# Optimization experiments

Hardware: AMD Instinct MI355X
Metric: run time of the kernel (lower is better)

## Reference

```python
import jax, jax.numpy as jnp
import numpy as np

B, N, D, H, K, L, BLOCKS = 8, 256, 768, 12, 128, 4, 2
HD = D // H
SCALING = HD ** -0.5
NEG = -1e9  # stand-in for -inf; exp underflows to exactly 0 in softmax


def layernorm(x, s, b):
    m = x.mean(-1, keepdims=True)
    v = ((x - m) ** 2).mean(-1, keepdims=True)
    return (x - m) * jax.lax.rsqrt(v + 1e-5) * s + b


def _gauss(x, mean, std):
    a = (2.0 * 3.14159) ** 0.5
    return jnp.exp(-0.5 * ((x - mean) / std) ** 2) / (a * std)


def setup_inputs() -> dict:
    key = jax.random.key(0)
    ks = jax.random.split(key, 16)
    nrm = lambda k, shape: jax.random.normal(k, shape, jnp.float32) * 0.02
    atoms = jax.random.randint(ks[0], (B, N), 0, 10, dtype=jnp.int32)
    pos = jax.random.normal(ks[1], (B, N, 3), jnp.float32)
    atom_emb = nrm(ks[2], (10, D)).at[0].set(0.0)  # padding_idx=0
    gbf_means = jax.random.uniform(ks[3], (K,), jnp.float32, 0.0, 3.0)
    gbf_stds = jax.random.uniform(ks[4], (K,), jnp.float32, 0.0, 3.0)
    gbf_mul = jnp.ones((100, 1), jnp.float32)
    gbf_bias = jnp.zeros((100, 1), jnp.float32)
    bp_w1 = nrm(ks[5], (K, K)); bp_b1 = jnp.zeros((K,), jnp.float32)
    bp_w2 = nrm(ks[6], (K, H)); bp_b2 = jnp.zeros((H,), jnp.float32)
    edge_w = nrm(ks[7], (K, D)); edge_b = jnp.zeros((D,), jnp.float32)
    ap_w = nrm(ks[8], (D, D)); ap_b = jnp.zeros((D,), jnp.float32)
    ln1_s = jnp.ones((L, D), jnp.float32); ln1_b = jnp.zeros((L, D), jnp.float32)
    wi = nrm(ks[9], (L, D, 3 * D)); bi = jnp.zeros((L, 3 * D), jnp.float32)
    wo = nrm(ks[10], (L, D, D)); bo = jnp.zeros((L, D), jnp.float32)
    ln2_s = jnp.ones((L, D), jnp.float32); ln2_b = jnp.zeros((L, D), jnp.float32)
    w1 = nrm(ks[11], (L, D, D)); b1 = jnp.zeros((L, D), jnp.float32)
    w2 = nrm(ks[12], (L, D, D)); b2 = jnp.zeros((L, D), jnp.float32)
    fln_s = jnp.ones((D,), jnp.float32); fln_b = jnp.zeros((D,), jnp.float32)
    return dict(atoms=atoms, pos=pos, atom_emb=atom_emb, gbf_means=gbf_means,
                gbf_stds=gbf_stds, gbf_mul=gbf_mul, gbf_bias=gbf_bias,
                bp_w1=bp_w1, bp_b1=bp_b1, bp_w2=bp_w2, bp_b2=bp_b2,
                edge_w=edge_w, edge_b=edge_b, ap_w=ap_w, ap_b=ap_b,
                ln1_s=ln1_s, ln1_b=ln1_b, wi=wi, bi=bi, wo=wo, bo=bo,
                ln2_s=ln2_s, ln2_b=ln2_b, w1=w1, b1=b1, w2=w2, b2=b2,
                fln_s=fln_s, fln_b=fln_b)


def reference(atoms, pos, atom_emb, gbf_means, gbf_stds, gbf_mul, gbf_bias,
              bp_w1, bp_b1, bp_w2, bp_b2, edge_w, edge_b, ap_w, ap_b,
              ln1_s, ln1_b, wi, bi, wo, bo, ln2_s, ln2_b, w1, b1, w2, b2,
              fln_s, fln_b):
    pad = atoms == 0  # [B,N]
    delta = pos[:, None, :, :] - pos[:, :, None, :]  # [B,N,N,3]
    sq = (delta * delta).sum(-1)
    dist = jnp.where(sq > 0, jnp.sqrt(jnp.where(sq > 0, sq, 1.0)), 0.0)  # safe sqrt
    et = atoms[:, :, None] * 10 + atoms[:, None, :]  # [B,N,N] in [0,100)
    e = gbf_mul[et] * dist[..., None] + gbf_bias[et]  # [B,N,N,1]
    gbf = _gauss(e, gbf_means, jnp.abs(gbf_stds) + 1e-5)  # [B,N,N,K]
    # zero out padded j-columns, sum over j -> per-node edge feature
    ef = jnp.where(pad[:, None, :, None], 0.0, gbf).sum(axis=2)  # [B,N,K]
    node = atom_emb[atoms] + ef @ edge_w + edge_b  # [B,N,D]
    x = jnp.swapaxes(node, 0, 1) @ ap_w + ap_b  # [N,B,D]
    # attention bias: K-dim Gaussian features -> per-head bias
    bias = jax.nn.gelu(gbf @ bp_w1 + bp_b1, approximate=False) @ bp_w2 + bp_b2  # [B,N,N,H]
    bias = jnp.transpose(bias, (0, 3, 1, 2))  # [B,H,N,N]
    bias = jnp.where(pad[:, None, None, :], NEG, bias)

    def body(x, p):
        s1, c1, Wi, Bi, Wo, Bo, s2, c2, W1, B1, W2, B2 = p
        h = layernorm(x, s1, c1)
        q, k, v = jnp.split(h @ Wi + Bi, 3, axis=-1)
        q = q.reshape(N, B, H, HD) * SCALING
        k = k.reshape(N, B, H, HD)
        v = v.reshape(N, B, H, HD)
        sc = jnp.einsum('ibhd,jbhd->bhij', q, k) + bias
        pA = jax.nn.softmax(sc, axis=-1)
        o = jnp.einsum('bhij,jbhd->ibhd', pA, v).reshape(N, B, D)
        x = x + o @ Wo + Bo
        h = layernorm(x, s2, c2)
        h = jax.nn.gelu(h @ W1 + B1, approximate=False) @ W2 + B2
        return x + h, None

    stacked = (ln1_s, ln1_b, wi, bi, wo, bo, ln2_s, ln2_b, w1, b1, w2, b2)
    for _ in range(BLOCKS):
        x, _ = jax.lax.scan(body, x, stacked)
    x = layernorm(x, fln_s, fln_b)
    return jnp.swapaxes(x, 0, 1)  # [B,N,D]
```

## Files before the change

### kernel.cpp

```cpp
#include <hip/hip_runtime.h>
#include <math.h>

constexpr int Bn = 8, Nn = 256, Dn = 768, Hn = 12, Kn = 128;
constexpr int Tn = Nn * Bn;
constexpr float SCALE = 0.125f;
constexpr float NEGB = -1e9f;
constexpr float INV768 = 1.0f / 768.0f;

typedef __attribute__((ext_vector_type(8))) short bf16x8;
typedef __attribute__((ext_vector_type(4))) float f32x4;

#define MFMA16(a, b, c) __builtin_amdgcn_mfma_f32_16x16x32_bf16((a), (b), (c), 0, 0, 0)

__device__ __forceinline__ void gload_lds16(const void* g, void* l) {
  __builtin_amdgcn_global_load_lds(
      (const __attribute__((address_space(1))) void*)g,
      (__attribute__((address_space(3))) void*)l, 16, 0, 0);
}

__device__ __forceinline__ ushort f2bf(float x) {
  union { float f; unsigned u; } v; v.f = x;
  unsigned r = (v.u + 0x7fff + ((v.u >> 16) & 1)) >> 16;
  return (ushort)r;
}
__device__ __forceinline__ ushort f2bf_t(float x) {
  union { float f; unsigned u; } v; v.f = x;
  return (ushort)(v.u >> 16);
}
__device__ __forceinline__ float bf2f(ushort u) {
  union { unsigned u; float f; } v; v.u = ((unsigned)u) << 16;
  return v.f;
}
__device__ __forceinline__ unsigned pk2(float a, float b) {
  return (unsigned)f2bf_t(a) | ((unsigned)f2bf_t(b) << 16);
}
__device__ __forceinline__ float gelu_fast(float x) {
  float u = x * (0.7978845608f + 0.0356774081f * x * x);
  float e = __expf(2.0f * u);
  float t = 1.0f - 2.0f / (e + 1.0f);
  return 0.5f * x * (1.0f + t);
}
__device__ __forceinline__ float wave_sum(float v) {
#pragma unroll
  for (int off = 32; off; off >>= 1) v += __shfl_xor(v, off);
  return v;
}

__global__ __launch_bounds__(256) void wtrans(const float* __restrict__ W,
                                              ushort* __restrict__ WT,
                                              int Kd, int Nd) {
  __shared__ float tile[64][65];
  const float* Wl = W + (size_t)blockIdx.z * Kd * Nd;
  ushort* WTl = WT + (size_t)blockIdx.z * Kd * Nd;
  int n0 = blockIdx.x * 64, k0 = blockIdx.y * 64;
  int tid = threadIdx.x;
  for (int e = tid; e < 64 * 64; e += 256) {
    int r = e >> 6, c = e & 63;
    tile[r][c] = Wl[(size_t)(k0 + r) * Nd + n0 + c];
  }
  __syncthreads();
  for (int e = tid; e < 64 * 64; e += 256) {
    int r = e >> 6, c = e & 63;
    WTl[(size_t)(n0 + r) * Kd + k0 + c] = f2bf(tile[c][r]);
  }
}

__global__ __launch_bounds__(256) void gbias_kernel(
    const int* __restrict__ atoms, const float* __restrict__ pos,
    const float* __restrict__ means, const float* __restrict__ stds,
    const float* __restrict__ gmul, const float* __restrict__ gbias_,
    const ushort* __restrict__ w1T, const float* __restrict__ b1,
    const float* __restrict__ w2, const float* __restrict__ b2,
    ushort* __restrict__ biasb, ushort* __restrict__ efb) {
  int i = blockIdx.x, b = blockIdx.y;
  __shared__ char W1s[32768];
  __shared__ char Ag[16384];
  __shared__ char W2s[4096];
  __shared__ float sj[256];
  __shared__ int pml[256];
  __shared__ float b1s[128], kA[128], kB[128], kC[128], kcns[128];
  const int tid = threadIdx.x, w = tid >> 6, ln = tid & 63;
  const int frow = ln & 15, fgrp = ln >> 4;
  {
    int srow = ln >> 4, sc = ln & 15;
#pragma unroll
    for (int q = 0; q < 8; ++q) {
      int inst = w * 8 + q;
      int row = inst * 4 + srow;
      const char* g = (const char*)(w1T + row * 128) + ((sc * 16) ^ ((row & 7) << 4));
      gload_lds16(g, W1s + inst * 1024);
    }
  }
  if (tid < 128) {
    float mean = means[tid];
    float sd = fabsf(stds[tid]) + 1e-5f;
    float inv = 1.0f / sd;
    float A = -0.5f * inv * inv;
    kA[tid] = A;
    kB[tid] = -2.0f * A * mean;
    kC[tid] = A * mean * mean;
    kcns[tid] = inv * 0.3989423f;
    b1s[tid] = b1[tid];
  }
  for (int e = tid; e < 2048; e += 256) {
    int h = e >> 7, k = e & 127;
    float v = (h < 12) ? w2[k * 12 + h] : 0.f;
    *(ushort*)(W2s + h * 256 + ((2 * k) ^ ((h & 7) << 4))) = f2bf(v);
  }
  {
    int ai = atoms[b * Nn + i];
    int j = tid;
    int aj = atoms[b * Nn + j];
    float dx = pos[(b * Nn + i) * 3]     - pos[(b * Nn + j) * 3];
    float dy = pos[(b * Nn + i) * 3 + 1] - pos[(b * Nn + j) * 3 + 1];
    float dz = pos[(b * Nn + i) * 3 + 2] - pos[(b * Nn + j) * 3 + 2];
    float sq = dx * dx + dy * dy + dz * dz;
    float d = sq > 0.f ? sqrtf(sq) : 0.f;
    int et = ai * 10 + aj;
    sj[j] = fmaf(gmul[et], d, gbias_[et]);
    pml[j] = (aj == 0);
  }
  __syncthreads();

  const int kp = tid & 63, rquad = tid >> 6;
  const int k0i = 2 * kp, k1i = 2 * kp + 1;
  const float A0 = kA[k0i], B0 = kB[k0i], C0 = kC[k0i], cn0 = kcns[k0i];
  const float A1 = kA[k1i], B1 = kB[k1i], C1 = kC[k1i], cn1 = kcns[k1i];
  float facc0 = 0.f, facc1 = 0.f;

  for (int jt = 0; jt < 4; ++jt) {
    int j0 = jt * 64;
#pragma unroll
    for (int rr = 0; rr < 16; ++rr) {
      int row = rquad * 16 + rr;
      int jg = j0 + row;
      float s = sj[jg];
      float e0 = __expf(fmaf(fmaf(A0, s, B0), s, C0));
      float e1 = __expf(fmaf(fmaf(A1, s, B1), s, C1));
      int padj = pml[jg];
      facc0 += padj ? 0.f : e0;
      facc1 += padj ? 0.f : e1;
      *(unsigned*)(Ag + row * 256 + ((4 * kp) ^ ((row & 7) << 4))) = pk2(e0 * cn0, e1 * cn1);
    }
    __syncthreads();
    f32x4 acc[8] = {};
    const int arow = w * 16 + frow;
#pragma unroll
    for (int ks = 0; ks < 4; ++ks) {
      bf16x8 af = *(const bf16x8*)(Ag + arow * 256 + ((ks * 64 + fgrp * 16) ^ ((arow & 7) << 4)));
#pragma unroll
      for (int nt = 0; nt < 8; ++nt) {
        int brow = nt * 16 + frow;
        bf16x8 bfv = *(const bf16x8*)(W1s + brow * 256 + ((ks * 64 + fgrp * 16) ^ ((brow & 7) << 4)));
        acc[nt] = MFMA16(af, bfv, acc[nt]);
      }
    }
    __syncthreads();
#pragma unroll
    for (int nt = 0; nt < 8; ++nt) {
      int n = nt * 16 + frow;
#pragma unroll
      for (int r = 0; r < 4; ++r) {
        int jloc = w * 16 + fgrp * 4 + r;
        float g = gelu_fast(acc[nt][r] + b1s[n]);
        *(ushort*)(Ag + jloc * 256 + ((2 * n) ^ ((jloc & 7) << 4))) = f2bf_t(g);
      }
    }
    __syncthreads();
    {
      f32x4 acc2 = {};
      int jrow = w * 16 + frow;
#pragma unroll
      for (int ks = 0; ks < 4; ++ks) {
        bf16x8 af = *(const bf16x8*)(Ag + jrow * 256 + ((ks * 64 + fgrp * 16) ^ ((jrow & 7) << 4)));
        bf16x8 bfv = *(const bf16x8*)(W2s + frow * 256 + ((ks * 64 + fgrp * 16) ^ ((frow & 7) << 4)));
        acc2 = MFMA16(af, bfv, acc2);
      }
      if (frow < 12) {
        float bv = b2[frow];
#pragma unroll
        for (int r = 0; r < 4; ++r) {
          int jl = w * 16 + fgrp * 4 + r;
          int jg = j0 + jl;
          float v = pml[jg] ? NEGB : (acc2[r] + bv);
          biasb[(((size_t)b * Hn + frow) * Nn + i) * Nn + jg] = f2bf(v);
        }
      }
    }
    __syncthreads();
  }
  {
    float* efp = (float*)Ag;
    efp[(kp * 4 + rquad) * 2 + 0] = facc0;
    efp[(kp * 4 + rquad) * 2 + 1] = facc1;
    __syncthreads();
    if (tid < 128) {
      int k = tid, kq = k >> 1, lo = k & 1;
      float s = efp[(kq * 4 + 0) * 2 + lo] + efp[(kq * 4 + 1) * 2 + lo] +
                efp[(kq * 4 + 2) * 2 + lo] + efp[(kq * 4 + 3) * 2 + lo];
      efb[(size_t)(b * Nn + i) * Kn + k] = f2bf(s * kcns[k]);
    }
  }
}

template <int MODE>
__global__ __launch_bounds__(256, 4) void mgemm(
    const ushort* __restrict__ A, const ushort* __restrict__ WT,
    const float* __restrict__ bias, const float* __restrict__ res,
    void* __restrict__ Cout, const int* __restrict__ atomsp,
    const float* __restrict__ embp, int M, int Kd, int Nd) {
  __shared__ char smem[16384];
  char* ldsA = smem;
  char* ldsB = smem + 8192;
  const int tid = threadIdx.x, w = tid >> 6, ln = tid & 63;
  const int m0 = blockIdx.y * 64, n0 = blockIdx.x * 64;
  const int wm = (w >> 1) * 32, wn = (w & 1) * 32;
  const int srow = ln >> 3, schunk = ln & 7;
  const int sswz = (schunk * 16) ^ (srow << 4);
  const int frow = ln & 15, fgrp = ln >> 4;
  f32x4 acc[2][2] = {};
  for (int kt = 0; kt < Kd; kt += 64) {
    __syncthreads();
#pragma unroll
    for (int q = 0; q < 2; ++q) {
      int r = (w * 2 + q) * 8 + srow;
      gload_lds16((const char*)(A + (size_t)(m0 + r) * Kd + kt) + sswz, ldsA + (w * 2 + q) * 1024);
    }
#pragma unroll
    for (int q = 0; q < 2; ++q) {
      int r = (w * 2 + q) * 8 + srow;
      gload_lds16((const char*)(WT + (size_t)(n0 + r) * Kd + kt) + sswz, ldsB + (w * 2 + q) * 1024);
    }
    __syncthreads();
#pragma unroll
    for (int ks = 0; ks < 2; ++ks) {
      bf16x8 af[2], bfv[2];
#pragma unroll
      for (int mt = 0; mt < 2; ++mt) {
        int row = wm + mt * 16 + frow;
        af[mt] = *(const bf16x8*)(ldsA + row * 128 + ((ks * 64 + fgrp * 16) ^ ((row & 7) << 4)));
      }
#pragma unroll
      for (int nt = 0; nt < 2; ++nt) {
        int row = wn + nt * 16 + frow;
        bfv[nt] = *(const bf16x8*)(ldsB + row * 128 + ((ks * 64 + fgrp * 16) ^ ((row & 7) << 4)));
      }
      acc[0][0] = MFMA16(af[0], bfv[0], acc[0][0]);
      acc[0][1] = MFMA16(af[0], bfv[1], acc[0][1]);
      acc[1][0] = MFMA16(af[1], bfv[0], acc[1][0]);
      acc[1][1] = MFMA16(af[1], bfv[1], acc[1][1]);
    }
  }
#pragma unroll
  for (int nt = 0; nt < 2; ++nt) {
    int n = n0 + wn + nt * 16 + frow;
    float bv = bias[n];
#pragma unroll
    for (int mt = 0; mt < 2; ++mt) {
#pragma unroll
      for (int r = 0; r < 4; ++r) {
        int m = m0 + wm + mt * 16 + fgrp * 4 + r;
        float v = acc[mt][nt][r] + bv;
        if (MODE == 1) v = gelu_fast(v);
        if (MODE == 2) v += res[(size_t)m * Nd + n];
        if (MODE == 5) v += embp[(size_t)atomsp[m] * Nd + n];
        if (MODE == 2 || MODE == 3) ((float*)Cout)[(size_t)m * Nd + n] = v;
        else                        ((ushort*)Cout)[(size_t)m * Nd + n] = f2bf(v);
      }
    }
  }
}

__global__ __launch_bounds__(256, 2) void mgemm128_qkv(
    const ushort* __restrict__ A, const ushort* __restrict__ WT,
    const float* __restrict__ bias, ushort* __restrict__ vTout,
    ushort* __restrict__ Cout, int M, int Kd, int Nd) {
  __shared__ char smem[32768];
  char* ldsA = smem;
  char* ldsB = smem + 16384;
  const int tid = threadIdx.x, w = tid >> 6, ln = tid & 63;
  const int m0 = blockIdx.y * 128, n0 = blockIdx.x * 128;
  const int wm = (w >> 1) * 64, wn = (w & 1) * 64;
  const int srow = ln >> 3, schunk = ln & 7;
  const int sswz = (schunk * 16) ^ (srow << 4);
  const int frow = ln & 15, fgrp = ln >> 4;
  f32x4 acc[4][4] = {};
  for (int kt = 0; kt < Kd; kt += 64) {
    __syncthreads();
#pragma unroll
    for (int q = 0; q < 4; ++q) {
      int r = (w * 4 + q) * 8 + srow;
      gload_lds16((const char*)(A + (size_t)(m0 + r) * Kd + kt) + sswz, ldsA + (w * 4 + q) * 1024);
    }
#pragma unroll
    for (int q = 0; q < 4; ++q) {
      int r = (w * 4 + q) * 8 + srow;
      gload_lds16((const char*)(WT + (size_t)(n0 + r) * Kd + kt) + sswz, ldsB + (w * 4 + q) * 1024);
    }
    __syncthreads();
#pragma unroll
    for (int ks = 0; ks < 2; ++ks) {
      bf16x8 af[4], bfv[4];
#pragma unroll
      for (int mt = 0; mt < 4; ++mt) {
        int row = wm + mt * 16 + frow;
        af[mt] = *(const bf16x8*)(ldsA + row * 128 + ((ks * 64 + fgrp * 16) ^ ((row & 7) << 4)));
      }
#pragma unroll
      for (int nt = 0; nt < 4; ++nt) {
        int row = wn + nt * 16 + frow;
        bfv[nt] = *(const bf16x8*)(ldsB + row * 128 + ((ks * 64 + fgrp * 16) ^ ((row & 7) << 4)));
      }
#pragma unroll
      for (int mt = 0; mt < 4; ++mt)
#pragma unroll
        for (int nt = 0; nt < 4; ++nt)
          acc[mt][nt] = MFMA16(af[mt], bfv[nt], acc[mt][nt]);
    }
  }
#pragma unroll
  for (int nt = 0; nt < 4; ++nt) {
    int n = n0 + wn + nt * 16 + frow;
    float bv = bias[n];
    if (n >= 1536) {
      int dd = n - 1536, h = dd >> 6, d = dd & 63;
#pragma unroll
      for (int mt = 0; mt < 4; ++mt) {
#pragma unroll
        for (int r = 0; r < 4; ++r) {
          int m = m0 + wm + mt * 16 + fgrp * 4 + r;
          int bb = m >> 8, j = m & 255;
          vTout[(((size_t)bb * Hn + h) * 64 + d) * 256 + j] = f2bf(acc[mt][nt][r] + bv);
        }
      }
    } else {
      float sc = (n < 768) ? SCALE : 1.0f;
#pragma unroll
      for (int mt = 0; mt < 4; ++mt) {
#pragma unroll
        for (int r = 0; r < 4; ++r) {
          int m = m0 + wm + mt * 16 + fgrp * 4 + r;
          Cout[(size_t)m * Nd + n] = f2bf((acc[mt][nt][r] + bv) * sc);
        }
      }
    }
  }
}

__global__ __launch_bounds__(256, 2) void attn_mfma(
    const ushort* __restrict__ qkv, const ushort* __restrict__ vT,
    const ushort* __restrict__ biasb, ushort* __restrict__ Oout) {
  int it = blockIdx.x, h = blockIdx.y, b = blockIdx.z;
  int i0 = it * 64;
  __shared__ char smem[65536];
  char* Ks = smem;
  char* Vs = smem + 32768;
  const int tid = threadIdx.x, w = tid >> 6, ln = tid & 63;
  const int frow = ln & 15, fgrp = ln >> 4;
  {
    const int srow = ln >> 3, schunk = ln & 7;
#pragma unroll
    for (int q = 0; q < 8; ++q) {
      int inst = w * 8 + q;
      int row = inst * 8 + srow;
      const char* g = (const char*)(qkv + (size_t)(b * Nn + row) * 2304 + 768 + h * 64) +
                      ((schunk * 16) ^ ((row & 7) << 4));
      gload_lds16(g, Ks + inst * 1024);
    }
#pragma unroll
    for (int q = 0; q < 8; ++q) {
      int inst = w * 8 + q;
      int row = inst * 2 + (ln >> 5);
      int cb = (ln & 31) * 16;
      const char* g = (const char*)(vT + (size_t)((b * Hn + h) * 64 + row) * 256) +
                      (cb ^ ((row & 7) << 4));
      gload_lds16(g, Vs + inst * 1024);
    }
  }
  bf16x8 qf[2];
  {
    int qrow = i0 + w * 16 + frow;
    const ushort* qg = qkv + (size_t)(b * Nn + qrow) * 2304 + h * 64 + fgrp * 8;
    qf[0] = *(const bf16x8*)qg;
    qf[1] = *(const bf16x8*)(qg + 32);
  }
  __syncthreads();
  f32x4 s[16];
#pragma unroll
  for (int jtl = 0; jtl < 16; ++jtl) {
    int row = jtl * 16 + frow;
    const char* kb = Ks + row * 128;
    bf16x8 k0 = *(const bf16x8*)(kb + ((fgrp * 16) ^ ((row & 7) << 4)));
    bf16x8 k1 = *(const bf16x8*)(kb + ((64 + fgrp * 16) ^ ((row & 7) << 4)));
    f32x4 t = {};
    t = MFMA16(qf[0], k0, t);
    t = MFMA16(qf[1], k1, t);
    s[jtl] = t;
  }
  float inv[4];
#pragma unroll
  for (int r = 0; r < 4; ++r) {
    int i = i0 + w * 16 + fgrp * 4 + r;
    const ushort* brow = biasb + (((size_t)b * Hn + h) * Nn + i) * Nn;
    float su = 0.f;
#pragma unroll
    for (int jtl = 0; jtl < 16; ++jtl) {
      float p = __expf(s[jtl][r] + bf2f(brow[jtl * 16 + frow]));
      s[jtl][r] = p;
      su += p;
    }
    su += __shfl_xor(su, 1); su += __shfl_xor(su, 2);
    su += __shfl_xor(su, 4); su += __shfl_xor(su, 8);
    inv[r] = 1.0f / su;
  }
  __syncthreads();
  char* Ps = Ks + w * 8192;
#pragma unroll
  for (int r = 0; r < 4; ++r) {
    int prow = fgrp * 4 + r;
#pragma unroll
    for (int jtl = 0; jtl < 16; ++jtl) {
      int cb = jtl * 32 + frow * 2;
      *(ushort*)(Ps + prow * 512 + (cb ^ ((prow & 7) << 4))) = f2bf_t(s[jtl][r]);
    }
  }
  __syncthreads();
  bf16x8 pf[8];
#pragma unroll
  for (int ks = 0; ks < 8; ++ks)
    pf[ks] = *(const bf16x8*)(Ps + frow * 512 + ((ks * 64 + fgrp * 16) ^ ((frow & 7) << 4)));
  f32x4 o[4] = {};
#pragma unroll
  for (int dt = 0; dt < 4; ++dt) {
#pragma unroll
    for (int ks = 0; ks < 8; ++ks) {
      int row = dt * 16 + frow;
      bf16x8 vf = *(const bf16x8*)(Vs + row * 512 + ((ks * 64 + fgrp * 16) ^ ((row & 7) << 4)));
      o[dt] = MFMA16(pf[ks], vf, o[dt]);
    }
  }
#pragma unroll
  for (int dt = 0; dt < 4; ++dt)
#pragma unroll
    for (int r = 0; r < 4; ++r) {
      int i = i0 + w * 16 + fgrp * 4 + r;
      Oout[(size_t)(b * Nn + i) * Dn + h * 64 + dt * 16 + frow] = f2bf(o[dt][r] * inv[r]);
    }
}

template <int MODE>
__global__ __launch_bounds__(256) void ln_kernel(
    const float* __restrict__ x, const float* __restrict__ sc,
    const float* __restrict__ bi, void* __restrict__ out) {
  int t = blockIdx.x;
  int tid = threadIdx.x;
  const float* xr = x + (size_t)t * Dn;
  float v0 = xr[tid], v1 = xr[tid + 256], v2 = xr[tid + 512];
  __shared__ float red[4], red2[4];
  float s = wave_sum(v0 + v1 + v2);
  if ((tid & 63) == 0) red[tid >> 6] = s;
  __syncthreads();
  float mean = (red[0] + red[1] + red[2] + red[3]) * INV768;
  float d0 = v0 - mean, d1 = v1 - mean, d2 = v2 - mean;
  float vs = wave_sum(d0 * d0 + d1 * d1 + d2 * d2);
  if ((tid & 63) == 0) red2[tid >> 6] = vs;
  __syncthreads();
  float var = (red2[0] + red2[1] + red2[2] + red2[3]) * INV768;
  float r = rsqrtf(var + 1e-5f);
  if (MODE == 0) {
    ushort* o = (ushort*)out + (size_t)t * Dn;
    o[tid]       = f2bf(d0 * r * sc[tid]       + bi[tid]);
    o[tid + 256] = f2bf(d1 * r * sc[tid + 256] + bi[tid + 256]);
    o[tid + 512] = f2bf(d2 * r * sc[tid + 512] + bi[tid + 512]);
  } else {
    float* o = (float*)out + (size_t)t * Dn;
    o[tid]       = d0 * r * sc[tid]       + bi[tid];
    o[tid + 256] = d1 * r * sc[tid + 256] + bi[tid + 256];
    o[tid + 512] = d2 * r * sc[tid + 512] + bi[tid + 512];
  }
}

extern "C" void kernel_launch(void* const* d_in, const int* in_sizes, int n_in,
                              void* d_out, int out_size, void* d_ws, size_t ws_size,
                              hipStream_t stream) {
  (void)in_sizes; (void)n_in; (void)out_size; (void)ws_size;
  const int*   atoms    = (const int*)  d_in[0];
  const float* pos      = (const float*)d_in[1];
  const float* atom_emb = (const float*)d_in[2];
  const float* gbf_means= (const float*)d_in[3];
  const float* gbf_stds = (const float*)d_in[4];
  const float* gbf_mul  = (const float*)d_in[5];
  const float* gbf_bias = (const float*)d_in[6];
  const float* bp_w1    = (const float*)d_in[7];
  const float* bp_b1    = (const float*)d_in[8];
  const float* bp_w2    = (const float*)d_in[9];
  const float* bp_b2    = (const float*)d_in[10];
  const float* edge_w   = (const float*)d_in[11];
  const float* edge_b   = (const float*)d_in[12];
  const float* ap_w     = (const float*)d_in[13];
  const float* ap_b     = (const float*)d_in[14];
  const float* ln1_s    = (const float*)d_in[15];
  const float* ln1_b    = (const float*)d_in[16];
  const float* wi       = (const float*)d_in[17];
  const float* bi       = (const float*)d_in[18];
  const float* wo       = (const float*)d_in[19];
  const float* bo       = (const float*)d_in[20];
  const float* ln2_s    = (const float*)d_in[21];
  const float* ln2_b    = (const float*)d_in[22];
  const float* w1       = (const float*)d_in[23];
  const float* b1       = (const float*)d_in[24];
  const float* w2       = (const float*)d_in[25];
  const float* b2       = (const float*)d_in[26];
  const float* fln_s    = (const float*)d_in[27];
  const float* fln_b    = (const float*)d_in[28];
  float* out = (float*)d_out;

  ushort* wsb   = (ushort*)d_ws;
  ushort* biasb = wsb;
  ushort* qkvb  = biasb + (size_t)Bn * Hn * Nn * Nn;
  ushort* hb    = qkvb + (size_t)Tn * 2304;
  ushort* vT    = hb + (size_t)Tn * Dn;
  ushort* wiT   = vT + (size_t)Bn * Hn * 64 * 256;
  ushort* woT   = wiT + (size_t)4 * 2304 * Dn;
  ushort* w1T   = woT + (size_t)4 * Dn * Dn;
  ushort* w2T   = w1T + (size_t)4 * Dn * Dn;
  ushort* w1bT  = w2T + (size_t)4 * Dn * Dn;
  float*  xbuf  = (float*)(w1bT + 16384);
  ushort* apT   = qkvb;
  ushort* ewT   = qkvb + 589824;
  ushort* ffnb  = qkvb;
  ushort* efb   = vT;

  wtrans<<<dim3(12, 12, 1), 256, 0, stream>>>(ap_w, apT, 768, 768);
  wtrans<<<dim3(36, 12, 4), 256, 0, stream>>>(wi, wiT, 768, 2304);
  wtrans<<<dim3(12, 12, 4), 256, 0, stream>>>(wo, woT, 768, 768);
  wtrans<<<dim3(12, 12, 4), 256, 0, stream>>>(w1, w1T, 768, 768);
  wtrans<<<dim3(12, 12, 4), 256, 0, stream>>>(w2, w2T, 768, 768);
  wtrans<<<dim3(2, 2, 1), 256, 0, stream>>>(bp_w1, w1bT, 128, 128);
  wtrans<<<dim3(12, 2, 1), 256, 0, stream>>>(edge_w, ewT, 128, 768);

  dim3 gridNB(Nn, Bn);
  gbias_kernel<<<gridNB, 256, 0, stream>>>(atoms, pos, gbf_means, gbf_stds,
                                           gbf_mul, gbf_bias, w1bT, bp_b1, bp_w2, bp_b2,
                                           biasb, efb);
  mgemm<5><<<dim3(12, 32), 256, 0, stream>>>(efb, ewT, edge_b, nullptr, hb,
                                             atoms, atom_emb, Tn, 128, Dn);
  mgemm<3><<<dim3(12, 32), 256, 0, stream>>>(hb, apT, ap_b, nullptr, xbuf,
                                             nullptr, nullptr, Tn, Dn, Dn);

  for (int it = 0; it < 8; ++it) {
    int l = it & 3;
    ln_kernel<0><<<Tn, 256, 0, stream>>>(xbuf, ln1_s + l * Dn, ln1_b + l * Dn, hb);
    mgemm128_qkv<<<dim3(18, 16), 256, 0, stream>>>(hb, wiT + (size_t)l * 2304 * Dn,
                                                   bi + l * 2304, vT, qkvb, Tn, Dn, 2304);
    attn_mfma<<<dim3(4, Hn, Bn), 256, 0, stream>>>(qkvb, vT, biasb, hb);
    mgemm<2><<<dim3(12, 32), 256, 0, stream>>>(hb, woT + (size_t)l * Dn * Dn,
                                               bo + l * Dn, xbuf, xbuf,
                                               nullptr, nullptr, Tn, Dn, Dn);
    ln_kernel<0><<<Tn, 256, 0, stream>>>(xbuf, ln2_s + l * Dn, ln2_b + l * Dn, hb);
    mgemm<1><<<dim3(12, 32), 256, 0, stream>>>(hb, w1T + (size_t)l * Dn * Dn,
                                               b1 + l * Dn, nullptr, ffnb,
                                               nullptr, nullptr, Tn, Dn, Dn);
    mgemm<2><<<dim3(12, 32), 256, 0, stream>>>(ffnb, w2T + (size_t)l * Dn * Dn,
                                               b2 + l * Dn, xbuf, xbuf,
                                               nullptr, nullptr, Tn, Dn, Dn);
  }
  ln_kernel<1><<<Tn, 256, 0, stream>>>(xbuf, fln_s, fln_b, out);
}
```

Measured before the change: 728.9 us.

## Merge weight transposes into one launch and split gbias j-tiles across two warp groups

```diff
diff --git a/kernel.cpp b/kernel.cpp
--- a/kernel.cpp
+++ b/kernel.cpp
@@ -46,26 +46,54 @@
   return v;
 }
 
-__global__ __launch_bounds__(256) void wtrans(const float* __restrict__ W,
-                                              ushort* __restrict__ WT,
-                                              int Kd, int Nd) {
+__global__ __launch_bounds__(256) void wtrans_all(
+    const float* __restrict__ ap_w, const float* __restrict__ wi,
+    const float* __restrict__ wo, const float* __restrict__ w1,
+    const float* __restrict__ w2, const float* __restrict__ bp_w1,
+    const float* __restrict__ edge_w,
+    ushort* __restrict__ apT, ushort* __restrict__ wiT, ushort* __restrict__ woT,
+    ushort* __restrict__ w1T, ushort* __restrict__ w2T, ushort* __restrict__ w1bT,
+    ushort* __restrict__ ewT) {
   __shared__ float tile[64][65];
-  const float* Wl = W + (size_t)blockIdx.z * Kd * Nd;
-  ushort* WTl = WT + (size_t)blockIdx.z * Kd * Nd;
-  int n0 = blockIdx.x * 64, k0 = blockIdx.y * 64;
+  int bid = blockIdx.x;
+  const float* W; ushort* WT; int Kd, Nd, nx;
+  if (bid < 144) { W = ap_w; WT = apT; Kd = 768; Nd = 768; nx = 12; }
+  else if ((bid -= 144) < 1728) {
+    int z = bid / 432; bid %= 432;
+    W = wi + (size_t)z * 768 * 2304; WT = wiT + (size_t)z * 768 * 2304;
+    Kd = 768; Nd = 2304; nx = 36;
+  }
+  else if ((bid -= 1728) < 576) {
+    int z = bid / 144; bid %= 144;
+    W = wo + (size_t)z * 768 * 768; WT = woT + (size_t)z * 768 * 768;
+    Kd = 768; Nd = 768; nx = 12;
+  }
+  else if ((bid -= 576) < 576) {
+    int z = bid / 144; bid %= 144;
+    W = w1 + (size_t)z * 768 * 768; WT = w1T + (size_t)z * 768 * 768;
+    Kd = 768; Nd = 768; nx = 12;
+  }
+  else if ((bid -= 576) < 576) {
+    int z = bid / 144; bid %= 144;
+    W = w2 + (size_t)z * 768 * 768; WT = w2T + (size_t)z * 768 * 768;
+    Kd = 768; Nd = 768; nx = 12;
+  }
+  else if ((bid -= 576) < 4) { W = bp_w1; WT = w1bT; Kd = 128; Nd = 128; nx = 2; }
+  else { bid -= 4; W = edge_w; WT = ewT; Kd = 128; Nd = 768; nx = 12; }
+  int n0 = (bid % nx) * 64, k0 = (bid / nx) * 64;
   int tid = threadIdx.x;
   for (int e = tid; e < 64 * 64; e += 256) {
     int r = e >> 6, c = e & 63;
-    tile[r][c] = Wl[(size_t)(k0 + r) * Nd + n0 + c];
+    tile[r][c] = W[(size_t)(k0 + r) * Nd + n0 + c];
   }
   __syncthreads();
   for (int e = tid; e < 64 * 64; e += 256) {
     int r = e >> 6, c = e & 63;
-    WTl[(size_t)(n0 + r) * Kd + k0 + c] = f2bf(tile[c][r]);
-  }
-}
-
-__global__ __launch_bounds__(256) void gbias_kernel(
+    WT[(size_t)(n0 + r) * Kd + k0 + c] = f2bf(tile[c][r]);
+  }
+}
+
+__global__ __launch_bounds__(512) void gbias_kernel(
     const int* __restrict__ atoms, const float* __restrict__ pos,
     const float* __restrict__ means, const float* __restrict__ stds,
     const float* __restrict__ gmul, const float* __restrict__ gbias_,
@@ -74,18 +102,23 @@
     ushort* __restrict__ biasb, ushort* __restrict__ efb) {
   int i = blockIdx.x, b = blockIdx.y;
   __shared__ char W1s[32768];
-  __shared__ char Ag[16384];
+  __shared__ char Ag[2][16384];
   __shared__ char W2s[4096];
   __shared__ float sj[256];
   __shared__ int pml[256];
   __shared__ float b1s[128], kA[128], kB[128], kC[128], kcns[128];
-  const int tid = threadIdx.x, w = tid >> 6, ln = tid & 63;
+  const int tid = threadIdx.x;
+  const int w = tid >> 6, ln = tid & 63;
+  const int grp = tid >> 8;
+  const int t256 = tid & 255;
+  const int wg = w & 3;
   const int frow = ln & 15, fgrp = ln >> 4;
+  char* myAg = Ag[grp];
   {
     int srow = ln >> 4, sc = ln & 15;
 #pragma unroll
-    for (int q = 0; q < 8; ++q) {
-      int inst = w * 8 + q;
+    for (int q = 0; q < 4; ++q) {
+      int inst = w * 4 + q;
       int row = inst * 4 + srow;
       const char* g = (const char*)(w1T + row * 128) + ((sc * 16) ^ ((row & 7) << 4));
       gload_lds16(g, W1s + inst * 1024);
@@ -102,12 +135,12 @@
     kcns[tid] = inv * 0.3989423f;
     b1s[tid] = b1[tid];
   }
-  for (int e = tid; e < 2048; e += 256) {
+  for (int e = tid; e < 2048; e += 512) {
     int h = e >> 7, k = e & 127;
     float v = (h < 12) ? w2[k * 12 + h] : 0.f;
     *(ushort*)(W2s + h * 256 + ((2 * k) ^ ((h & 7) << 4))) = f2bf(v);
   }
-  {
+  if (tid < 256) {
     int ai = atoms[b * Nn + i];
     int j = tid;
     int aj = atoms[b * Nn + j];
@@ -122,13 +155,14 @@
   }
   __syncthreads();
 
-  const int kp = tid & 63, rquad = tid >> 6;
+  const int kp = t256 & 63, rquad = t256 >> 6;
   const int k0i = 2 * kp, k1i = 2 * kp + 1;
   const float A0 = kA[k0i], B0 = kB[k0i], C0 = kC[k0i], cn0 = kcns[k0i];
   const float A1 = kA[k1i], B1 = kB[k1i], C1 = kC[k1i], cn1 = kcns[k1i];
   float facc0 = 0.f, facc1 = 0.f;
 
-  for (int jt = 0; jt < 4; ++jt) {
+  for (int tt = 0; tt < 2; ++tt) {
+    int jt = grp * 2 + tt;
     int j0 = jt * 64;
 #pragma unroll
     for (int rr = 0; rr < 16; ++rr) {
@@ -140,14 +174,14 @@
       int padj = pml[jg];
       facc0 += padj ? 0.f : e0;
       facc1 += padj ? 0.f : e1;
-      *(unsigned*)(Ag + row * 256 + ((4 * kp) ^ ((row & 7) << 4))) = pk2(e0 * cn0, e1 * cn1);
+      *(unsigned*)(myAg + row * 256 + ((4 * kp) ^ ((row & 7) << 4))) = pk2(e0 * cn0, e1 * cn1);
     }
     __syncthreads();
     f32x4 acc[8] = {};
-    const int arow = w * 16 + frow;
+    const int arow = wg * 16 + frow;
 #pragma unroll
     for (int ks = 0; ks < 4; ++ks) {
-      bf16x8 af = *(const bf16x8*)(Ag + arow * 256 + ((ks * 64 + fgrp * 16) ^ ((arow & 7) << 4)));
+      bf16x8 af = *(const bf16x8*)(myAg + arow * 256 + ((ks * 64 + fgrp * 16) ^ ((arow & 7) << 4)));
 #pragma unroll
       for (int nt = 0; nt < 8; ++nt) {
         int brow = nt * 16 + frow;
@@ -161,18 +195,18 @@
       int n = nt * 16 + frow;
 #pragma unroll
       for (int r = 0; r < 4; ++r) {
-        int jloc = w * 16 + fgrp * 4 + r;
+        int jloc = wg * 16 + fgrp * 4 + r;
         float g = gelu_fast(acc[nt][r] + b1s[n]);
-        *(ushort*)(Ag + jloc * 256 + ((2 * n) ^ ((jloc & 7) << 4))) = f2bf_t(g);
+        *(ushort*)(myAg + jloc * 256 + ((2 * n) ^ ((jloc & 7) << 4))) = f2bf_t(g);
       }
     }
     __syncthreads();
     {
       f32x4 acc2 = {};
-      int jrow = w * 16 + frow;
+      int jrow = wg * 16 + frow;
 #pragma unroll
       for (int ks = 0; ks < 4; ++ks) {
-        bf16x8 af = *(const bf16x8*)(Ag + jrow * 256 + ((ks * 64 + fgrp * 16) ^ ((jrow & 7) << 4)));
+        bf16x8 af = *(const bf16x8*)(myAg + jrow * 256 + ((ks * 64 + fgrp * 16) ^ ((jrow & 7) << 4)));
         bf16x8 bfv = *(const bf16x8*)(W2s + frow * 256 + ((ks * 64 + fgrp * 16) ^ ((frow & 7) << 4)));
         acc2 = MFMA16(af, bfv, acc2);
       }
@@ -180,7 +214,7 @@
         float bv = b2[frow];
 #pragma unroll
         for (int r = 0; r < 4; ++r) {
-          int jl = w * 16 + fgrp * 4 + r;
+          int jl = wg * 16 + fgrp * 4 + r;
           int jg = j0 + jl;
           float v = pml[jg] ? NEGB : (acc2[r] + bv);
           biasb[(((size_t)b * Hn + frow) * Nn + i) * Nn + jg] = f2bf(v);
@@ -190,14 +224,15 @@
     __syncthreads();
   }
   {
-    float* efp = (float*)Ag;
-    efp[(kp * 4 + rquad) * 2 + 0] = facc0;
-    efp[(kp * 4 + rquad) * 2 + 1] = facc1;
+    float* efp = (float*)Ag[0];
+    efp[(kp * 8 + grp * 4 + rquad) * 2 + 0] = facc0;
+    efp[(kp * 8 + grp * 4 + rquad) * 2 + 1] = facc1;
     __syncthreads();
     if (tid < 128) {
       int k = tid, kq = k >> 1, lo = k & 1;
-      float s = efp[(kq * 4 + 0) * 2 + lo] + efp[(kq * 4 + 1) * 2 + lo] +
-                efp[(kq * 4 + 2) * 2 + lo] + efp[(kq * 4 + 3) * 2 + lo];
+      float s = 0.f;
+#pragma unroll
+      for (int q = 0; q < 8; ++q) s += efp[(kq * 8 + q) * 2 + lo];
       efb[(size_t)(b * Nn + i) * Kn + k] = f2bf(s * kcns[k]);
     }
   }
@@ -531,16 +566,11 @@
   ushort* ffnb  = qkvb;
   ushort* efb   = vT;
 
-  wtrans<<<dim3(12, 12, 1), 256, 0, stream>>>(ap_w, apT, 768, 768);
-  wtrans<<<dim3(36, 12, 4), 256, 0, stream>>>(wi, wiT, 768, 2304);
-  wtrans<<<dim3(12, 12, 4), 256, 0, stream>>>(wo, woT, 768, 768);
-  wtrans<<<dim3(12, 12, 4), 256, 0, stream>>>(w1, w1T, 768, 768);
-  wtrans<<<dim3(12, 12, 4), 256, 0, stream>>>(w2, w2T, 768, 768);
-  wtrans<<<dim3(2, 2, 1), 256, 0, stream>>>(bp_w1, w1bT, 128, 128);
-  wtrans<<<dim3(12, 2, 1), 256, 0, stream>>>(edge_w, ewT, 128, 768);
+  wtrans_all<<<3628, 256, 0, stream>>>(ap_w, wi, wo, w1, w2, bp_w1, edge_w,
+                                       apT, wiT, woT, w1T, w2T, w1bT, ewT);
 
   dim3 gridNB(Nn, Bn);
-  gbias_kernel<<<gridNB, 256, 0, stream>>>(atoms, pos, gbf_means, gbf_stds,
+  gbias_kernel<<<gridNB, 512, 0, stream>>>(atoms, pos, gbf_means, gbf_stds,
                                            gbf_mul, gbf_bias, w1bT, bp_b1, bp_w2, bp_b2,
                                            biasb, efb);
   mgemm<5><<<dim3(12, 32), 256, 0, stream>>>(efb, ewT, edge_b, nullptr, hb,
```

Result: no change. 729.2 us (+0.0%).
